# Performance work log

Measured on AMD Instinct MI355X. Metric: run time of the kernel, lower is better.

## Reference

```python
import jax, jax.numpy as jnp
import numpy as np

MAX_HOPS = 2
N_NODES = 100000
N_EDGES = 1600000
D_FEAT = 64

def setup_inputs() -> dict:
    key = jax.random.key(0)
    k1, k2 = jax.random.split(key)
    x = jax.random.normal(k1, (N_NODES, D_FEAT), dtype=jnp.float32)
    edge_index = jax.random.randint(k2, (2, N_EDGES), 0, N_NODES, dtype=jnp.int64)
    hop_weights = jnp.ones((MAX_HOPS + 1,), dtype=jnp.float32)
    return {"x": x, "edge_index": edge_index, "hop_weights": hop_weights}

def reference(x, edge_index, hop_weights):
    num_nodes = x.shape[0]
    loops = jnp.arange(num_nodes, dtype=edge_index.dtype)
    row = jnp.concatenate([edge_index[0], loops])  # destination of scatter-add
    col = jnp.concatenate([edge_index[1], loops])  # gather source
    # symmetric GCN normalization D^{-1/2} A D^{-1/2} (degree computed over col, as in source)
    deg = jax.ops.segment_sum(jnp.ones_like(col, dtype=x.dtype), col, num_segments=num_nodes)
    deg_inv_sqrt = jnp.where(deg > 0, jax.lax.rsqrt(deg), 0.0)
    norm = deg_inv_sqrt[row] * deg_inv_sqrt[col]  # [E+N]
    w = jax.nn.softmax(hop_weights)
    result = w[0] * x
    current = x
    for hop in range(1, MAX_HOPS + 1):
        messages = current[col] * norm[:, None]  # irregular gather + scale
        current = jax.ops.segment_sum(messages, row, num_segments=num_nodes)  # scatter-add
        result = result + w[hop] * current
    return result
```

## Files before the change

### kernel.cpp

```cpp
#include <hip/hip_runtime.h>

#define NN 100000
#define NE 1600000
#define D 64

#define BKT 256
#define BROWS ((NN + BKT - 1) / BKT)
#define CAP 8192
#define PADCAP 12288
#define P1_NB 512
#define P1_T 1024
#define EPB ((NE + P1_NB - 1) / P1_NB)

typedef unsigned short u16;
typedef unsigned int u32;
typedef unsigned char u8;
typedef __attribute__((ext_vector_type(8))) unsigned short us8;


__device__ __forceinline__ float bf2f(u16 u) {
    union { u32 i; float f; } x; x.i = ((u32)u) << 16; return x.f;
}
__device__ __forceinline__ u16 f2bf(float f) {
    union { float f; u32 i; } x; x.f = f;
    u32 r = x.i + 0x7FFF + ((x.i >> 16) & 1);
    return (u16)(r >> 16);
}

__global__ void setup_kernel(const float* __restrict__ hw, float* __restrict__ wsm,
                             int* __restrict__ bcnt, int* __restrict__ bcnt2) {
    int t = threadIdx.x;
    if (t < BKT) bcnt[t] = 0;
    else if (t < 2 * BKT) bcnt2[t - BKT] = 0;
    else if (t == 2 * BKT) {
        float m = fmaxf(fmaxf(hw[0], hw[1]), hw[2]);
        float e0 = expf(hw[0] - m), e1 = expf(hw[1] - m), e2 = expf(hw[2] - m);
        float s = e0 + e1 + e2;
        wsm[0] = e0 / s; wsm[1] = e1 / s; wsm[2] = e2 / s;
    }
}

__global__ void __launch_bounds__(P1_T) fused_p1(const int* __restrict__ row,
                                                 const int* __restrict__ col,
                                                 int* __restrict__ bcnt,
                                                 int* __restrict__ bcnt2,
                                                 u32* __restrict__ buck,
                                                 u16* __restrict__ buck2) {
    __shared__ int lds_r[EPB];
    __shared__ int lds_c[EPB];
    __shared__ u32 st1[EPB];
    __shared__ u16 st2[EPB];
    __shared__ u8  sb1[EPB];
    __shared__ u8  sb2[EPB];
    __shared__ int h[BKT], h2[BKT];
    __shared__ int hoff[BKT], hoff2[BKT];
    __shared__ int resv[BKT], resv2[BKT];
    int t = threadIdx.x;
    int beg = blockIdx.x * EPB, end = min(NE, beg + EPB);
    int n = end - beg;
    for (int i = t; i < BKT; i += P1_T) { h[i] = 0; h2[i] = 0; }
    __syncthreads();
    for (int i = t; i < n; i += P1_T) {
        int r = row[beg + i], c = col[beg + i];
        lds_r[i] = r; lds_c[i] = c;
        atomicAdd(&h[r / BROWS], 1);
        atomicAdd(&h2[c / BROWS], 1);
    }
    __syncthreads();
    int id = t & 255;
    int side = t >> 8;
    int* arr = (side == 0) ? h : h2;
    int myc = (side < 2) ? arr[id] : 0;
    for (int st = 1; st < BKT; st <<= 1) {
        int u = 0;
        if (side < 2 && id >= st) u = arr[id - st];
        __syncthreads();
        if (side < 2) arr[id] += u;
        __syncthreads();
    }
    if (side == 0) {
        hoff[id] = h[id] - myc;
        resv[id] = atomicAdd(&bcnt[id], myc);
    } else if (side == 1) {
        hoff2[id] = h2[id] - myc;
        resv2[id] = atomicAdd(&bcnt2[id], myc);
    }
    __syncthreads();
    if (t < BKT) h[t] = hoff[t];
    else if (t < 2 * BKT) h2[t - BKT] = hoff2[t - BKT];
    __syncthreads();
    for (int i = t; i < n; i += P1_T) {
        int r = lds_r[i], c = lds_c[i];
        int b1 = r / BROWS;
        int pos = atomicAdd(&h[b1], 1);
        st1[pos] = ((u32)(r - b1 * BROWS) << 17) | (u32)c;
        sb1[pos] = (u8)b1;
        int b2 = c / BROWS;
        int pos2 = atomicAdd(&h2[b2], 1);
        st2[pos2] = (u16)(c - b2 * BROWS);
        sb2[pos2] = (u8)b2;
    }
    __syncthreads();
    for (int i = t; i < n; i += P1_T) {
        int b1 = sb1[i];
        buck[(size_t)b1 * CAP + resv[b1] + (i - hoff[b1])] = st1[i];
        int b2 = sb2[i];
        buck2[(size_t)b2 * CAP + resv2[b2] + (i - hoff2[b2])] = st2[i];
    }
}

__global__ void __launch_bounds__(1024) deg_scale(const int* __restrict__ bcnt2,
                                                  const u16* __restrict__ buck2,
                                                  float* __restrict__ dis,
                                                  float* __restrict__ dsi,
                                                  const float4* __restrict__ x,
                                                  ushort4* __restrict__ y1,
                                                  ushort4* __restrict__ y2) {
    __shared__ int ca[BROWS];
    int b = blockIdx.x, t = threadIdx.x;
    int row0 = b * BROWS;
    int nrows = min(BROWS, NN - row0);
    int cntb = bcnt2[b];
    const u16* eb = buck2 + (size_t)b * CAP;
    for (int i = t; i < nrows; i += 1024) ca[i] = 0;
    __syncthreads();
    for (int e = t; e < cntb; e += 1024)
        atomicAdd(&ca[eb[e]], 1);
    __syncthreads();
    if (t < nrows) {
        float dg = (float)(ca[t] + 1);
        dis[row0 + t] = rsqrtf(dg);
        dsi[row0 + t] = sqrtf(dg);
    }
    int items = nrows * 16;
    for (int i = t; i < items; i += 1024) {
        int r = i >> 4;
        float s = rsqrtf((float)(ca[r] + 1));
        int gidx = (row0 + r) * 16 + (i & 15);
        float4 v = x[gidx];
        ushort4 o;
        o.x = f2bf(s * v.x); o.y = f2bf(s * v.y); o.z = f2bf(s * v.z); o.w = f2bf(s * v.w);
        y1[gidx] = o;
    }
    if (b == BKT - 1 && t < 16) {
        ushort4 z = {0, 0, 0, 0};
        y1[NN * 16 + t] = z;
        y2[NN * 16 + t] = z;
    }
}

__global__ void __launch_bounds__(1024) p2_build(const int* __restrict__ bcnt,
                                                 const u32* __restrict__ buck,
                                                 int* __restrict__ adjc,
                                                 int2* __restrict__ rowbe) {
    __shared__ int ca[BROWS];
    __shared__ int wsum[16];
    int b = blockIdx.x, t = threadIdx.x;
    int row0 = b * BROWS;
    int nrows = min(BROWS, NN - row0);
    int cntb = bcnt[b];
    const u32* eb = buck + (size_t)b * CAP;

    for (int i = t; i < nrows; i += 1024) ca[i] = 0;
    __syncthreads();
    for (int e = t; e < cntb; e += 1024)
        atomicAdd(&ca[eb[e] >> 17], 1);
    __syncthreads();
    int v = (t < nrows) ? ca[t] : 0;
    int vp = (v + 15) & ~15;
    int lane = t & 63, wv = t >> 6;
    int incl = vp;
    #pragma unroll
    for (int d = 1; d < 64; d <<= 1) {
        int u = __shfl_up(incl, d);
        if (lane >= d) incl += u;
    }
    if (lane == 63) wsum[wv] = incl;
    __syncthreads();
    if (t < 16) {
        int s = wsum[t];
        #pragma unroll
        for (int d = 1; d < 16; d <<= 1) {
            int u = __shfl_up(s, d, 16);
            if (t >= d) s += u;
        }
        wsum[t] = s;
    }
    __syncthreads();
    int excl = ((wv > 0) ? wsum[wv - 1] : 0) + incl - vp;
    if (t < nrows) {
        int base = b * PADCAP + excl;
        rowbe[row0 + t] = make_int2(base, base + vp);
        for (int p = base + v; p < base + vp; ++p) adjc[p] = NN;
        ca[t] = base;
    }
    __syncthreads();
    for (int e = t; e < cntb; e += 1024) {
        u32 p = eb[e];
        int pos = atomicAdd(&ca[p >> 17], 1);
        adjc[pos] = (int)(p & 0x1FFFFu);
    }
}


__global__ void prop1_kernel(const int2* __restrict__ rowbe,
                             const int* __restrict__ adjc,
                             const float* __restrict__ dis,
                             const u16* __restrict__ y1,
                             u16* __restrict__ y2) {
    int tid = blockIdx.x * blockDim.x + threadIdx.x;
    int w = tid >> 6, l = tid & 63;
    int n = 2 * w + (l >> 5);
    int sg = (l >> 3) & 3;
    int ho = l & 7;
    int2 be = rowbe[n];
    float a[8] = {0.f, 0.f, 0.f, 0.f, 0.f, 0.f, 0.f, 0.f};
    #pragma unroll 2
    for (int j = be.x; j < be.y; j += 16) {
        int4 c = *(const int4*)&adjc[j + sg * 4];
        us8 v0 = *(const us8*)&y1[c.x * D + ho * 8];
        us8 v1 = *(const us8*)&y1[c.y * D + ho * 8];
        us8 v2 = *(const us8*)&y1[c.z * D + ho * 8];
        us8 v3 = *(const us8*)&y1[c.w * D + ho * 8];
        #pragma unroll
        for (int k = 0; k < 8; ++k)
            a[k] += (bf2f(v0[k]) + bf2f(v1[k])) + (bf2f(v2[k]) + bf2f(v3[k]));
    }
    #pragma unroll
    for (int k = 0; k < 8; ++k) {
        a[k] += __shfl_xor(a[k], 8);
        a[k] += __shfl_xor(a[k], 16);
    }
    if ((l & 31) < 8) {
        us8 s = *(const us8*)&y1[n * D + ho * 8];
        float di = dis[n], d2 = di * di;
        us8 o;
        #pragma unroll
        for (int k = 0; k < 8; ++k) o[k] = f2bf(d2 * (a[k] + bf2f(s[k])));
        *(us8*)&y2[n * D + ho * 8] = o;
    }
}

__global__ void prop2_kernel(const int2* __restrict__ rowbe,
                             const int* __restrict__ adjc,
                             const float* __restrict__ dis,
                             const float* __restrict__ dsi,
                             const u16* __restrict__ y1,
                             const u16* __restrict__ y2,
                             const float* __restrict__ wsm,
                             float* __restrict__ out) {
    int tid = blockIdx.x * blockDim.x + threadIdx.x;
    int w = tid >> 6, l = tid & 63;
    int n = 2 * w + (l >> 5);
    int sg = (l >> 3) & 3;
    int ho = l & 7;
    int2 be = rowbe[n];
    float a[8] = {0.f, 0.f, 0.f, 0.f, 0.f, 0.f, 0.f, 0.f};
    #pragma unroll 2
    for (int j = be.x; j < be.y; j += 16) {
        int4 c = *(const int4*)&adjc[j + sg * 4];
        us8 v0 = *(const us8*)&y2[c.x * D + ho * 8];
        us8 v1 = *(const us8*)&y2[c.y * D + ho * 8];
        us8 v2 = *(const us8*)&y2[c.z * D + ho * 8];
        us8 v3 = *(const us8*)&y2[c.w * D + ho * 8];
        #pragma unroll
        for (int k = 0; k < 8; ++k)
            a[k] += (bf2f(v0[k]) + bf2f(v1[k])) + (bf2f(v2[k]) + bf2f(v3[k]));
    }
    #pragma unroll
    for (int k = 0; k < 8; ++k) {
        a[k] += __shfl_xor(a[k], 8);
        a[k] += __shfl_xor(a[k], 16);
    }
    if ((l & 31) < 8) {
        us8 s1 = *(const us8*)&y1[n * D + ho * 8];
        us8 s2 = *(const us8*)&y2[n * D + ho * 8];
        float di = dis[n], ds = dsi[n];
        float w0 = wsm[0], w1 = wsm[1], w2 = wsm[2];
        float o[8];
        #pragma unroll
        for (int k = 0; k < 8; ++k) {
            float y2k = bf2f(s2[k]);
            o[k] = ds * (w0 * bf2f(s1[k]) + w1 * y2k) + w2 * (di * (a[k] + y2k));
        }
        float4 o0 = {o[0], o[1], o[2], o[3]};
        float4 o1 = {o[4], o[5], o[6], o[7]};
        *(float4*)&out[n * D + ho * 8] = o0;
        *(float4*)&out[n * D + ho * 8 + 4] = o1;
    }
}


extern "C" void kernel_launch(void* const* d_in, const int* in_sizes, int n_in,
                              void* d_out, int out_size, void* d_ws, size_t ws_size,
                              hipStream_t stream) {
    const float* x   = (const float*)d_in[0];
    const int*   ei  = (const int*)d_in[1];
    const float* hw  = (const float*)d_in[2];
    float*       out = (float*)d_out;

    const int* row = ei;
    const int* col = ei + NE;

    char* ws = (char*)d_ws;
    size_t off = 0;
    auto alloc = [&](size_t bytes) { size_t p = off; off += (bytes + 255) & ~(size_t)255; return p; };
    float* wsm    = (float*)(ws + alloc(16));
    int*   bcnt   = (int*)  (ws + alloc((size_t)BKT * 4));
    int*   bcnt2  = (int*)  (ws + alloc((size_t)BKT * 4));
    float* dis    = (float*)(ws + alloc((size_t)NN * 4));
    float* dsi    = (float*)(ws + alloc((size_t)NN * 4));
    u32*   buck   = (u32*)  (ws + alloc((size_t)BKT * CAP * 4));
    u16*   buck2  = (u16*)  (ws + alloc((size_t)BKT * CAP * 2));
    int*   adjc   = (int*)  (ws + alloc((size_t)BKT * PADCAP * 4));
    int2*  rowbe  = (int2*) (ws + alloc((size_t)NN * 8));
    u16*   y1     = (u16*)  (ws + alloc((size_t)(NN + 1) * D * 2));
    u16*   y2     = (u16*)  (ws + alloc((size_t)(NN + 1) * D * 2));

    setup_kernel<<<1, 1024, 0, stream>>>(hw, wsm, bcnt, bcnt2);
    fused_p1<<<P1_NB, P1_T, 0, stream>>>(row, col, bcnt, bcnt2, buck, buck2);
    deg_scale<<<BKT, 1024, 0, stream>>>(bcnt2, buck2, dis, dsi,
                                        (const float4*)x, (ushort4*)y1, (ushort4*)y2);
    p2_build<<<BKT, 1024, 0, stream>>>(bcnt, buck, adjc, rowbe);

    const int prop_blocks = (NN / 2 + 3) / 4;
    prop1_kernel<<<prop_blocks, 256, 0, stream>>>(rowbe, adjc, dis, y1, y2);
    prop2_kernel<<<prop_blocks, 256, 0, stream>>>(rowbe, adjc, dis, dsi, y1, y2, wsm, out);
}
```

Before: 117.0 us.

## Merge degree-scale and CSR build kernels; shrink p1 blocks and drop LDS edge staging

Combines the deg_scale and p2_build launches into a single 512-block kernel, with blocks split by index between the two independent jobs, so they run concurrently and one launch boundary disappears. The bucketing pass now uses 1024 blocks of 512 threads. It no longer stages row/col in shared memory and instead re-reads them from global memory in the scatter pass. This cuts LDS use per block, which may allow more resident blocks, at the cost of a second global read of the edge lists.

New measurement: 124.5 us. 6.4% more time.

```diff
diff --git a/kernel.cpp b/kernel.cpp
--- a/kernel.cpp
+++ b/kernel.cpp
@@ -8,8 +8,8 @@
 #define BROWS ((NN + BKT - 1) / BKT)
 #define CAP 8192
 #define PADCAP 12288
-#define P1_NB 512
-#define P1_T 1024
+#define P1_NB 1024
+#define P1_T 512
 #define EPB ((NE + P1_NB - 1) / P1_NB)
 
 typedef unsigned short u16;
@@ -46,8 +46,6 @@
                                                  int* __restrict__ bcnt2,
                                                  u32* __restrict__ buck,
                                                  u16* __restrict__ buck2) {
-    __shared__ int lds_r[EPB];
-    __shared__ int lds_c[EPB];
     __shared__ u32 st1[EPB];
     __shared__ u16 st2[EPB];
     __shared__ u8  sb1[EPB];
@@ -61,36 +59,33 @@
     for (int i = t; i < BKT; i += P1_T) { h[i] = 0; h2[i] = 0; }
     __syncthreads();
     for (int i = t; i < n; i += P1_T) {
-        int r = row[beg + i], c = col[beg + i];
-        lds_r[i] = r; lds_c[i] = c;
-        atomicAdd(&h[r / BROWS], 1);
-        atomicAdd(&h2[c / BROWS], 1);
+        atomicAdd(&h[row[beg + i] / BROWS], 1);
+        atomicAdd(&h2[col[beg + i] / BROWS], 1);
     }
     __syncthreads();
     int id = t & 255;
     int side = t >> 8;
     int* arr = (side == 0) ? h : h2;
-    int myc = (side < 2) ? arr[id] : 0;
+    int myc = arr[id];
     for (int st = 1; st < BKT; st <<= 1) {
-        int u = 0;
-        if (side < 2 && id >= st) u = arr[id - st];
-        __syncthreads();
-        if (side < 2) arr[id] += u;
+        int u = (id >= st) ? arr[id - st] : 0;
+        __syncthreads();
+        arr[id] += u;
         __syncthreads();
     }
     if (side == 0) {
         hoff[id] = h[id] - myc;
         resv[id] = atomicAdd(&bcnt[id], myc);
-    } else if (side == 1) {
+    } else {
         hoff2[id] = h2[id] - myc;
         resv2[id] = atomicAdd(&bcnt2[id], myc);
     }
     __syncthreads();
     if (t < BKT) h[t] = hoff[t];
-    else if (t < 2 * BKT) h2[t - BKT] = hoff2[t - BKT];
+    else h2[t - BKT] = hoff2[t - BKT];
     __syncthreads();
     for (int i = t; i < n; i += P1_T) {
-        int r = lds_r[i], c = lds_c[i];
+        int r = row[beg + i], c = col[beg + i];
         int b1 = r / BROWS;
         int pos = atomicAdd(&h[b1], 1);
         st1[pos] = ((u32)(r - b1 * BROWS) << 17) | (u32)c;
@@ -109,96 +104,96 @@
     }
 }
 
-__global__ void __launch_bounds__(1024) deg_scale(const int* __restrict__ bcnt2,
-                                                  const u16* __restrict__ buck2,
-                                                  float* __restrict__ dis,
-                                                  float* __restrict__ dsi,
-                                                  const float4* __restrict__ x,
-                                                  ushort4* __restrict__ y1,
-                                                  ushort4* __restrict__ y2) {
-    __shared__ int ca[BROWS];
-    int b = blockIdx.x, t = threadIdx.x;
-    int row0 = b * BROWS;
-    int nrows = min(BROWS, NN - row0);
-    int cntb = bcnt2[b];
-    const u16* eb = buck2 + (size_t)b * CAP;
-    for (int i = t; i < nrows; i += 1024) ca[i] = 0;
-    __syncthreads();
-    for (int e = t; e < cntb; e += 1024)
-        atomicAdd(&ca[eb[e]], 1);
-    __syncthreads();
-    if (t < nrows) {
-        float dg = (float)(ca[t] + 1);
-        dis[row0 + t] = rsqrtf(dg);
-        dsi[row0 + t] = sqrtf(dg);
-    }
-    int items = nrows * 16;
-    for (int i = t; i < items; i += 1024) {
-        int r = i >> 4;
-        float s = rsqrtf((float)(ca[r] + 1));
-        int gidx = (row0 + r) * 16 + (i & 15);
-        float4 v = x[gidx];
-        ushort4 o;
-        o.x = f2bf(s * v.x); o.y = f2bf(s * v.y); o.z = f2bf(s * v.z); o.w = f2bf(s * v.w);
-        y1[gidx] = o;
-    }
-    if (b == BKT - 1 && t < 16) {
-        ushort4 z = {0, 0, 0, 0};
-        y1[NN * 16 + t] = z;
-        y2[NN * 16 + t] = z;
-    }
-}
-
-__global__ void __launch_bounds__(1024) p2_build(const int* __restrict__ bcnt,
-                                                 const u32* __restrict__ buck,
-                                                 int* __restrict__ adjc,
-                                                 int2* __restrict__ rowbe) {
+__global__ void __launch_bounds__(1024) build_both(const int* __restrict__ bcnt,
+                                                   const u32* __restrict__ buck,
+                                                   int* __restrict__ adjc,
+                                                   int2* __restrict__ rowbe,
+                                                   const int* __restrict__ bcnt2,
+                                                   const u16* __restrict__ buck2,
+                                                   float* __restrict__ dis,
+                                                   float* __restrict__ dsi,
+                                                   const float4* __restrict__ x,
+                                                   ushort4* __restrict__ y1,
+                                                   ushort4* __restrict__ y2) {
     __shared__ int ca[BROWS];
     __shared__ int wsum[16];
-    int b = blockIdx.x, t = threadIdx.x;
-    int row0 = b * BROWS;
-    int nrows = min(BROWS, NN - row0);
-    int cntb = bcnt[b];
-    const u32* eb = buck + (size_t)b * CAP;
-
-    for (int i = t; i < nrows; i += 1024) ca[i] = 0;
-    __syncthreads();
-    for (int e = t; e < cntb; e += 1024)
-        atomicAdd(&ca[eb[e] >> 17], 1);
-    __syncthreads();
-    int v = (t < nrows) ? ca[t] : 0;
-    int vp = (v + 15) & ~15;
-    int lane = t & 63, wv = t >> 6;
-    int incl = vp;
-    #pragma unroll
-    for (int d = 1; d < 64; d <<= 1) {
-        int u = __shfl_up(incl, d);
-        if (lane >= d) incl += u;
-    }
-    if (lane == 63) wsum[wv] = incl;
-    __syncthreads();
-    if (t < 16) {
-        int s = wsum[t];
-        #pragma unroll
-        for (int d = 1; d < 16; d <<= 1) {
-            int u = __shfl_up(s, d, 16);
-            if (t >= d) s += u;
-        }
-        wsum[t] = s;
-    }
-    __syncthreads();
-    int excl = ((wv > 0) ? wsum[wv - 1] : 0) + incl - vp;
-    if (t < nrows) {
-        int base = b * PADCAP + excl;
-        rowbe[row0 + t] = make_int2(base, base + vp);
-        for (int p = base + v; p < base + vp; ++p) adjc[p] = NN;
-        ca[t] = base;
-    }
-    __syncthreads();
-    for (int e = t; e < cntb; e += 1024) {
-        u32 p = eb[e];
-        int pos = atomicAdd(&ca[p >> 17], 1);
-        adjc[pos] = (int)(p & 0x1FFFFu);
+    int t = threadIdx.x;
+    if (blockIdx.x < BKT) {
+        int b = blockIdx.x;
+        int row0 = b * BROWS;
+        int nrows = min(BROWS, NN - row0);
+        int cntb = bcnt2[b];
+        const u16* eb = buck2 + (size_t)b * CAP;
+        for (int i = t; i < nrows; i += 1024) ca[i] = 0;
+        __syncthreads();
+        for (int e = t; e < cntb; e += 1024)
+            atomicAdd(&ca[eb[e]], 1);
+        __syncthreads();
+        if (t < nrows) {
+            float dg = (float)(ca[t] + 1);
+            dis[row0 + t] = rsqrtf(dg);
+            dsi[row0 + t] = sqrtf(dg);
+        }
+        int items = nrows * 16;
+        for (int i = t; i < items; i += 1024) {
+            int r = i >> 4;
+            float s = rsqrtf((float)(ca[r] + 1));
+            int gidx = (row0 + r) * 16 + (i & 15);
+            float4 v = x[gidx];
+            ushort4 o;
+            o.x = f2bf(s * v.x); o.y = f2bf(s * v.y); o.z = f2bf(s * v.z); o.w = f2bf(s * v.w);
+            y1[gidx] = o;
+        }
+        if (b == BKT - 1 && t < 16) {
+            ushort4 z = {0, 0, 0, 0};
+            y1[NN * 16 + t] = z;
+            y2[NN * 16 + t] = z;
+        }
+    } else {
+        int b = blockIdx.x - BKT;
+        int row0 = b * BROWS;
+        int nrows = min(BROWS, NN - row0);
+        int cntb = bcnt[b];
+        const u32* eb = buck + (size_t)b * CAP;
+        for (int i = t; i < nrows; i += 1024) ca[i] = 0;
+        __syncthreads();
+        for (int e = t; e < cntb; e += 1024)
+            atomicAdd(&ca[eb[e] >> 17], 1);
+        __syncthreads();
+        int v = (t < nrows) ? ca[t] : 0;
+        int vp = (v + 15) & ~15;
+        int lane = t & 63, wv = t >> 6;
+        int incl = vp;
+        #pragma unroll
+        for (int d = 1; d < 64; d <<= 1) {
+            int u = __shfl_up(incl, d);
+            if (lane >= d) incl += u;
+        }
+        if (lane == 63) wsum[wv] = incl;
+        __syncthreads();
+        if (t < 16) {
+            int s = wsum[t];
+            #pragma unroll
+            for (int d = 1; d < 16; d <<= 1) {
+                int u = __shfl_up(s, d, 16);
+                if (t >= d) s += u;
+            }
+            wsum[t] = s;
+        }
+        __syncthreads();
+        int excl = ((wv > 0) ? wsum[wv - 1] : 0) + incl - vp;
+        if (t < nrows) {
+            int base = b * PADCAP + excl;
+            rowbe[row0 + t] = make_int2(base, base + vp);
+            for (int p = base + v; p < base + vp; ++p) adjc[p] = NN;
+            ca[t] = base;
+        }
+        __syncthreads();
+        for (int e = t; e < cntb; e += 1024) {
+            u32 p = eb[e];
+            int pos = atomicAdd(&ca[p >> 17], 1);
+            adjc[pos] = (int)(p & 0x1FFFFu);
+        }
     }
 }
 
@@ -319,9 +314,9 @@
 
     setup_kernel<<<1, 1024, 0, stream>>>(hw, wsm, bcnt, bcnt2);
     fused_p1<<<P1_NB, P1_T, 0, stream>>>(row, col, bcnt, bcnt2, buck, buck2);
-    deg_scale<<<BKT, 1024, 0, stream>>>(bcnt2, buck2, dis, dsi,
-                                        (const float4*)x, (ushort4*)y1, (ushort4*)y2);
-    p2_build<<<BKT, 1024, 0, stream>>>(bcnt, buck, adjc, rowbe);
+    build_both<<<2 * BKT, 1024, 0, stream>>>(bcnt, buck, adjc, rowbe,
+                                             bcnt2, buck2, dis, dsi,
+                                             (const float4*)x, (ushort4*)y1, (ushort4*)y2);
 
     const int prop_blocks = (NN / 2 + 3) / 4;
     prop1_kernel<<<prop_blocks, 256, 0, stream>>>(rowbe, adjc, dis, y1, y2);
```
